# Optimization experiments

Hardware: AMD Instinct MI355X
Metric: run time of the kernel (lower is better)

Reference implementation:

```python
import jax, jax.numpy as jnp
import numpy as np

NMS_THR = 0.7
TOPK = 128      # fixed post-NMS rois per level (static padding for jit)
OUT = 14        # RoIAlign output size
SAMPLES = 2     # samples per bin per dim (fixed approximation of sampling_ratio=-1)
STRIDES = (32.0, 16.0, 8.0)


def get_channel(a):
    # a: [..., 4] boxes as (cx, cy, w, h); FPN level assignment, clamped to [1, 4]
    s = jnp.sqrt(a[..., 2] * a[..., 3])
    return jnp.clip(jnp.floor(3.0 + jnp.log2(s / 224.0)), 1.0, 4.0)


def cxcywh_to_xyxy(b):
    cx, cy, w, h = b[..., 0], b[..., 1], b[..., 2], b[..., 3]
    return jnp.stack([cx - w / 2, cy - h / 2, cx + w / 2, cy + h / 2], axis=-1)


def pairwise_iou(b):
    x1, y1, x2, y2 = b[:, 0], b[:, 1], b[:, 2], b[:, 3]
    area = jnp.maximum(x2 - x1, 0.0) * jnp.maximum(y2 - y1, 0.0)
    ix1 = jnp.maximum(x1[:, None], x1[None, :])
    iy1 = jnp.maximum(y1[:, None], y1[None, :])
    ix2 = jnp.minimum(x2[:, None], x2[None, :])
    iy2 = jnp.minimum(y2[:, None], y2[None, :])
    inter = jnp.maximum(ix2 - ix1, 0.0) * jnp.maximum(iy2 - iy1, 0.0)
    union = area[:, None] + area[None, :] - inter
    return inter / jnp.maximum(union, 1e-9)


def nms_keep(boxes_xyxy, scores, thr):
    # Greedy NMS over masked scores (-inf entries sort last and are excluded later).
    n = scores.shape[0]
    order = jnp.argsort(-scores)
    iou = pairwise_iou(boxes_xyxy[order])  # [N, N]
    idx = jnp.arange(n)

    def body(sup, i):
        keep_i = ~sup[i]
        sup = sup | (keep_i & (iou[i] > thr) & (idx > i))
        return sup, keep_i

    _, keeps_sorted = jax.lax.scan(body, jnp.zeros(n, dtype=bool), idx)
    return jnp.zeros(n, dtype=bool).at[order].set(keeps_sorted)


def roi_align(feat, boxes):
    # feat: [C, H, W]; boxes: [K, 4]. NOTE: the original prepare_boxes feeds
    # (cx, cy, w, h) straight into RoIAlign, which interprets them as
    # (x1, y1, x2, y2) -- replicated faithfully here. spatial_scale = 1.
    C, H, W = feat.shape
    K = boxes.shape[0]
    x1, y1, x2, y2 = boxes[:, 0], boxes[:, 1], boxes[:, 2], boxes[:, 3]
    rw = jnp.maximum(x2 - x1, 1.0)
    rh = jnp.maximum(y2 - y1, 1.0)
    bw = rw / OUT
    bh = rh / OUT
    # fractional bin offsets, [OUT*SAMPLES]
    f = (jnp.arange(OUT, dtype=feat.dtype)[:, None]
         + (jnp.arange(SAMPLES, dtype=feat.dtype)[None, :] + 0.5) / SAMPLES).reshape(-1)
    ys = y1[:, None] + bh[:, None] * f[None, :]  # [K, S]
    xs = x1[:, None] + bw[:, None] * f[None, :]
    Y = ys[:, :, None]  # [K, S, 1]
    X = xs[:, None, :]  # [K, 1, S]
    valid = (Y > -1.0) & (Y < H) & (X > -1.0) & (X < W)  # [K, S, S]
    Yc = jnp.clip(Y, 0.0, H - 1.0)
    Xc = jnp.clip(X, 0.0, W - 1.0)
    y0 = jnp.floor(Yc)
    x0 = jnp.floor(Xc)
    y0i = y0.astype(jnp.int32)
    x0i = x0.astype(jnp.int32)
    y1i = jnp.minimum(y0i + 1, H - 1)
    x1i = jnp.minimum(x0i + 1, W - 1)
    ly = Yc - y0
    lx = Xc - x0
    hy = 1.0 - ly
    hx = 1.0 - lx
    g = lambda yi, xi: feat[:, yi, xi]  # -> [C, K, S, S]
    val = (g(y0i, x0i) * (hy * hx) + g(y0i, x1i) * (hy * lx)
           + g(y1i, x0i) * (ly * hx) + g(y1i, x1i) * (ly * lx))
    val = val * valid.astype(val.dtype)
    val = val.reshape(C, K, OUT, SAMPLES, OUT, SAMPLES).mean(axis=(3, 5))
    return jnp.transpose(val, (1, 0, 2, 3))  # [K, C, OUT, OUT]


def level_extract(feat, boxes, scores, levs, nl):
    # one image, one target FPN level: mask, NMS, fixed top-K select, RoIAlign
    mask = levs == nl
    msc = jnp.where(mask, scores, -jnp.inf)
    xyxy = cxcywh_to_xyxy(boxes)
    keep = nms_keep(jax.lax.stop_gradient(xyxy), jax.lax.stop_gradient(msc), NMS_THR)
    eff = jnp.where(keep & mask, msc, -jnp.inf)
    vals, sel = jax.lax.top_k(jax.lax.stop_gradient(eff), TOPK)
    valid = jnp.isfinite(vals)
    rois = boxes[sel] * valid[:, None].astype(boxes.dtype)
    out = roi_align(feat, rois)
    return out * valid[:, None, None, None].astype(out.dtype)


def _forward(p32, p16, p8, p4, a32, a16, a8, s32, s16, s8):
    anchors = (a32, a16, a8)  # p4 proposals are computed then discarded in the
    # original (grouping loop only runs l in range(3)); p4 features are never
    # RoIAligned either (nl loops 1..3), so p4 only appears as an unused input.
    levs = jnp.concatenate([get_channel(a) for a in anchors], axis=1)      # [B, N]
    boxes = jnp.concatenate([a * s for a, s in zip(anchors, STRIDES)], axis=1)
    scores = jnp.concatenate([s32, s16, s8], axis=1)
    outs = []
    for nl, feat in zip((1.0, 2.0, 3.0), (p32, p16, p8)):
        fn = jax.vmap(lambda f, b, s, l, nl=nl: level_extract(f, b, s, l, nl))
        outs.append(fn(feat, boxes, scores, levs))  # [B, TOPK, C, 14, 14]
    return jnp.concatenate(outs, axis=1)  # [B, 3*TOPK, C, 14, 14]


def setup_inputs():
    key = jax.random.key(0)
    ks = jax.random.split(key, 10)
    B, C = 2, 256
    p32 = jax.random.normal(ks[0], (B, C, 32, 32), jnp.float32)
    p16 = jax.random.normal(ks[1], (B, C, 64, 64), jnp.float32)
    p8 = jax.random.normal(ks[2], (B, C, 128, 128), jnp.float32)
    p4 = jax.random.normal(ks[3], (B, C, 256, 256), jnp.float32)

    def mk_anchors(k, n, hf):
        k1, k2 = jax.random.split(k)
        cxy = jax.random.uniform(k1, (B, n, 2), jnp.float32) * hf
        wh = 16.0 + jax.random.uniform(k2, (B, n, 2), jnp.float32) * 434.0
        return jnp.concatenate([cxy, wh], axis=-1)

    anchors_32 = mk_anchors(ks[4], 512, 32.0)
    anchors_16 = mk_anchors(ks[5], 1024, 64.0)
    anchors_8 = mk_anchors(ks[6], 2048, 128.0)
    scores_32 = jax.random.normal(ks[7], (B, 512), jnp.float32)
    scores_16 = jax.random.normal(ks[8], (B, 1024), jnp.float32)
    scores_8 = jax.random.normal(ks[9], (B, 2048), jnp.float32)
    return dict(p32=p32, p16=p16, p8=p8, p4=p4,
                anchors_32=anchors_32, anchors_16=anchors_16, anchors_8=anchors_8,
                scores_32=scores_32, scores_16=scores_16, scores_8=scores_8)


def reference(p32, p16, p8, p4, anchors_32, anchors_16, anchors_8,
              scores_32, scores_16, scores_8):
    return _forward(p32, p16, p8, p4, anchors_32, anchors_16, anchors_8,
                    scores_32, scores_16, scores_8)
```

## Files before the change

### kernel.cpp

```cpp
#include <hip/hip_runtime.h>
#include <stdint.h>

#define NMS_THR 0.7f
#define TOPK 128
#define NTOT 3584
#define CAP 2048
#define OUTSZ 14
#define NSAMP 28

typedef unsigned long long u64;
typedef float vf4 __attribute__((ext_vector_type(4)));
typedef float float2u __attribute__((ext_vector_type(2), aligned(4)));

__device__ __forceinline__ u64 shfl_xor64(u64 v, int mask) {
    int lo = __shfl_xor((int)(unsigned)v, mask);
    int hi = __shfl_xor((int)(v >> 32), mask);
    return ((u64)(unsigned)hi << 32) | (unsigned)lo;
}
__device__ __forceinline__ void cex_shfl(u64 &e, int t, int j, int k) {
    u64 p = shfl_xor64(e, j);
    bool up = ((t & k) == 0);
    bool lower = ((t & j) == 0);
    u64 mn = (e < p) ? e : p;
    u64 mx = (e < p) ? p : e;
    e = (lower == up) ? mn : mx;
}
__device__ __forceinline__ void cex_reg(u64 &a, u64 &b, int t, int k) {
    bool up = ((t & k) == 0);
    if ((a > b) == up) { u64 x = a; a = b; b = x; }
}
__device__ __forceinline__ float boxarea(float4 b) {
    return __fmul_rn(fmaxf(__fsub_rn(b.z, b.x), 0.0f),
                     fmaxf(__fsub_rn(b.w, b.y), 0.0f));
}
__device__ __forceinline__ bool iou_gt(float4 a, float aa, float4 b, float ba) {
    float i1 = fmaxf(a.x, b.x), i2 = fmaxf(a.y, b.y);
    float i3 = fminf(a.z, b.z), i4 = fminf(a.w, b.w);
    float inr = __fmul_rn(fmaxf(__fsub_rn(i3, i1), 0.0f),
                          fmaxf(__fsub_rn(i4, i2), 0.0f));
    float unr = __fsub_rn(__fadd_rn(aa, ba), inr);
    return __fdiv_rn(inr, fmaxf(unr, 1e-9f)) > NMS_THR;
}

__device__ __forceinline__ void fetch_anchor(
    const float* __restrict__ a32, const float* __restrict__ a16,
    const float* __restrict__ a8,
    const float* __restrict__ s32, const float* __restrict__ s16,
    const float* __restrict__ s8,
    int b, int i, float* A, float* st, float* sc)
{
    const float* P;
    if (i < 512) {
        P = a32 + (b * 512 + i) * 4;  *st = 32.0f; *sc = s32[b * 512 + i];
    } else if (i < 1536) {
        int j = i - 512;
        P = a16 + (b * 1024 + j) * 4; *st = 16.0f; *sc = s16[b * 1024 + j];
    } else {
        int j = i - 1536;
        P = a8 + (b * 2048 + j) * 4;  *st = 8.0f;  *sc = s8[b * 2048 + j];
    }
    float4 v = *(const float4*)P;
    A[0] = v.x; A[1] = v.y; A[2] = v.z; A[3] = v.w;
}

__global__ __launch_bounds__(1024) void select_kernel(
    const float* __restrict__ a32, const float* __restrict__ a16,
    const float* __restrict__ a8,
    const float* __restrict__ s32, const float* __restrict__ s16,
    const float* __restrict__ s8,
    float* __restrict__ rois,
    int* __restrict__ validOut)
{
    __shared__ u64 keys[CAP];
    __shared__ float4 cbox4[CAP];
    __shared__ float4 kb4[TOPK];
    __shared__ float karea[TOPK];
    __shared__ u64 extw[16];
    __shared__ int selList[TOPK];
    __shared__ int mCount, keptSh;

    int prob = blockIdx.x;
    int b = prob / 3;
    int nl = prob % 3 + 1;
    int tid = threadIdx.x;
    int lane = tid & 63;
    int wv = tid >> 6;
    int t0 = (wv << 7) + lane;
    int t1 = t0 + 64;

    if (tid == 0) mCount = 0;
    __syncthreads();

    for (int i = tid; i < NTOT; i += 1024) {
        float A[4], st, sc;
        fetch_anchor(a32, a16, a8, s32, s16, s8, b, i, A, &st, &sc);
        float s = sqrtf(__fmul_rn(A[2], A[3]));
        float lv = floorf(__fadd_rn(3.0f, log2f(__fdiv_rn(s, 224.0f))));
        lv = fminf(fmaxf(lv, 1.0f), 4.0f);
        bool sel = ((int)lv == nl);
        u64 bal = __ballot(sel);
        if (bal) {
            int pos0;
            if (lane == 0) pos0 = atomicAdd(&mCount, __popcll(bal));
            pos0 = __shfl(pos0, 0);
            if (sel) {
                unsigned u = __float_as_uint(sc);
                u = (u & 0x80000000u) ? ~u : (u | 0x80000000u);
                unsigned d = ~u;
                int pos = pos0 + __popcll(bal & ((1ull << lane) - 1ull));
                if (pos < CAP) keys[pos] = ((u64)d << 32) | (unsigned)i;
            }
        }
    }
    __syncthreads();
    int m = mCount;
    if (m > CAP) m = CAP;
    for (int i = m + tid; i < CAP; i += 1024) keys[i] = ~0ull;
    __syncthreads();

    {
        u64 e0 = keys[t0], e1 = keys[t1];
        for (int k = 2; k <= 128; k <<= 1) {
            int jstart = k >> 1;
            if (k == 128) {
                cex_reg(e0, e1, t0, k);
                jstart = 32;
            }
            for (int j = jstart; j > 0; j >>= 1) {
                cex_shfl(e0, t0, j, k);
                cex_shfl(e1, t1, j, k);
            }
        }
        keys[t0] = e0; keys[t1] = e1;
    }
    __syncthreads();
    for (int k = 256; k <= 2048; k <<= 1) {
        for (int j = k >> 1; j >= 128; j >>= 1) {
            for (int t = tid; t < CAP; t += 1024) {
                int ixj = t ^ j;
                if (ixj > t) {
                    u64 a = keys[t], bb = keys[ixj];
                    bool up = ((t & k) == 0);
                    if ((a > bb) == up) { keys[t] = bb; keys[ixj] = a; }
                }
            }
            __syncthreads();
        }
        {
            u64 e0 = keys[t0], e1 = keys[t1];
            cex_reg(e0, e1, t0, k);
            for (int j = 32; j > 0; j >>= 1) {
                cex_shfl(e0, t0, j, k);
                cex_shfl(e1, t1, j, k);
            }
            keys[t0] = e0; keys[t1] = e1;
        }
        __syncthreads();
    }

    for (int r = tid; r < m; r += 1024) {
        int orig = (int)(keys[r] & 0xffffffffu);
        float A[4], st, sc;
        fetch_anchor(a32, a16, a8, s32, s16, s8, b, orig, A, &st, &sc);
        float cx = A[0] * st, cy = A[1] * st, w = A[2] * st, h = A[3] * st;
        float4 v;
        v.x = __fsub_rn(cx, 0.5f * w);
        v.y = __fsub_rn(cy, 0.5f * h);
        v.z = __fadd_rn(cx, 0.5f * w);
        v.w = __fadd_rn(cy, 0.5f * h);
        cbox4[r] = v;
    }
    __syncthreads();

    int kept = 0;
    for (int base = 0; base < m && kept < TOPK; base += 64) {
        int n = m - base; if (n > 64) n = 64;
        bool cv = lane < n;
        float4 cb = cbox4[base + (cv ? lane : 0)];
        float car = boxarea(cb);

        bool s = false;
        for (int kk = wv; kk < kept; kk += 16)
            if (iou_gt(kb4[kk], karea[kk], cb, car)) s = true;
        u64 balA = __ballot(s && cv);
        if (lane == 0) extw[wv] = balA;
        __syncthreads();

        if (wv == 0) {
            u64 ext = extw[0] | extw[1] | extw[2]  | extw[3]
                    | extw[4] | extw[5] | extw[6]  | extw[7]
                    | extw[8] | extw[9] | extw[10] | extw[11]
                    | extw[12]| extw[13]| extw[14] | extw[15];
            bool alive = cv && !((ext >> lane) & 1ull);
            int nk = kept;
            while (nk < TOPK) {
                u64 bal = __ballot(alive);
                if (bal == 0ull) break;
                int pick = __builtin_ctzll(bal);
                float4 pb;
                pb.x = __shfl(cb.x, pick);
                pb.y = __shfl(cb.y, pick);
                pb.z = __shfl(cb.z, pick);
                pb.w = __shfl(cb.w, pick);
                float par = __shfl(car, pick);
                if (lane == 0) selList[nk] = base + pick;
                if (lane == 1) { kb4[nk] = pb; karea[nk] = par; }
                alive = alive && (lane != pick) && !iou_gt(pb, par, cb, car);
                nk++;
            }
            if (lane == 0) keptSh = nk;
        }
        __syncthreads();
        kept = keptSh;
    }

    for (int k = tid; k < TOPK; k += 1024) {
        float4 rv = make_float4(0.0f, 0.0f, 0.0f, 0.0f);
        int vld = 0;
        if (k < kept) {
            int orig = (int)(keys[selList[k]] & 0xffffffffu);
            float A[4], st, sc;
            fetch_anchor(a32, a16, a8, s32, s16, s8, b, orig, A, &st, &sc);
            rv = make_float4(A[0] * st, A[1] * st, A[2] * st, A[3] * st);
            vld = 1;
        }
        ((float4*)rois)[prob * TOPK + k] = rv;
        validOut[prob * TOPK + k] = vld;
    }
}

__global__ __launch_bounds__(256) void roialign_kernel(
    const float* __restrict__ p32, const float* __restrict__ p16,
    const float* __restrict__ p8,
    const float* __restrict__ rois, const int* __restrict__ validIn,
    float* __restrict__ out)
{
    int roiIdx = blockIdx.x;
    int b = roiIdx / 384;
    int slot = roiIdx - b * 384;
    int lvl = slot / TOPK;
    int k = slot - lvl * TOPK;
    int prob = b * 3 + lvl;
    int tid = threadIdx.x;

    float* O = out + (size_t)roiIdx * 256 * 196;

    vf4 z = (vf4)0.0f;
    vf4* O4 = (vf4*)O;
    for (int i = tid; i < 12544; i += 256) O4[i] = z;

    int vld = validIn[prob * TOPK + k];
    if (!vld) return;

    int W;
    const float* feat;
    if (lvl == 0)      { W = 32;  feat = p32; }
    else if (lvl == 1) { W = 64;  feat = p16; }
    else               { W = 128; feat = p8; }
    int HW = W * W;
    const float* F0 = feat + (size_t)b * 256 * HW;

    __shared__ int sxb[NSAMP], sy0[NSAMP], sy1[NSAMP];
    __shared__ float swx0[NSAMP], swx1[NSAMP], shy[NSAMP], sly[NSAMP];
    __shared__ int sxv[NSAMP], syv[NSAMP];
    __shared__ int oiL[OUTSZ], ojL[OUTSZ];
    __shared__ int nyx[2];

    if (tid < 2 * NSAMP) {
        const float* R = rois + ((size_t)prob * TOPK + k) * 4;
        float x1 = R[0], y1 = R[1], x2 = R[2], y2 = R[3];
        float rw = fmaxf(__fsub_rn(x2, x1), 1.0f);
        float rh = fmaxf(__fsub_rn(y2, y1), 1.0f);
        float bw = __fdiv_rn(rw, 14.0f);
        float bh = __fdiv_rn(rh, 14.0f);
        int axis = tid / NSAMP;
        int s = tid - axis * NSAMP;
        float fi = (float)(s >> 1) + ((s & 1) ? 0.75f : 0.25f);
        float start = axis ? y1 : x1;
        float bsz = axis ? bh : bw;
        float lim = (float)W;
        float X = __fadd_rn(start, __fmul_rn(bsz, fi));
        bool v = (X > -1.0f) && (X < lim);
        float Xc = fminf(fmaxf(X, 0.0f), lim - 1.0f);
        float x0f = floorf(Xc);
        int x0 = (int)x0f;
        float l = __fsub_rn(Xc, x0f);
        float hh = __fsub_rn(1.0f, l);
        float vf = v ? 1.0f : 0.0f;
        if (axis == 0) {
            int base; float w0, w1;
            if (x0 >= W - 1) { base = W - 2; w0 = 0.0f; w1 = vf; }
            else             { base = x0;    w0 = hh * vf; w1 = l * vf; }
            sxb[s] = base; swx0[s] = w0; swx1[s] = w1; sxv[s] = v ? 1 : 0;
        } else {
            sy0[s] = x0; sy1[s] = min(x0 + 1, W - 1);
            shy[s] = hh * vf; sly[s] = l * vf; syv[s] = v ? 1 : 0;
        }
    }
    __syncthreads();

    if (tid == 0) {
        int n = 0;
        for (int oi = 0; oi < OUTSZ; oi++)
            if (syv[2 * oi] | syv[2 * oi + 1]) oiL[n++] = oi;
        nyx[0] = n;
    }
    if (tid == 1) {
        int n = 0;
        for (int oj = 0; oj < OUTSZ; oj++)
            if (sxv[2 * oj] | sxv[2 * oj + 1]) ojL[n++] = oj;
        nyx[1] = n;
    }
    __syncthreads();

    int ny = nyx[0], nx = nyx[1];
    int total = ny * nx;
    if (total == 0) return;

    int w = tid >> 6;
    int lane = tid & 63;

    for (int ci = w; ci < total; ci += 4) {
        int oi = oiL[ci / nx];
        int oj = ojL[ci - (ci / nx) * nx];
        int sA = oi * 2, sB = sA + 1;
        int tA = oj * 2, tB = tA + 1;
        int y0A = sy0[sA], y1A = sy1[sA], y0B = sy0[sB], y1B = sy1[sB];
        float hyA = shy[sA], lyA = sly[sA], hyB = shy[sB], lyB = sly[sB];
        int xA = sxb[tA], xB = sxb[tB];
        float xw0A = swx0[tA], xw1A = swx1[tA];
        float xw0B = swx0[tB], xw1B = swx1[tB];
        int p = oi * 14 + oj;

        for (int it = 0; it < 4; it++) {
            int c = lane + it * 64;
            const float* F = F0 + c * HW;
            const float* rA0 = F + y0A * W;
            const float* rA1 = F + y1A * W;
            const float* rB0 = F + y0B * W;
            const float* rB1 = F + y1B * W;

            float2u a0 = *(const float2u*)(rA0 + xA);
            float2u a1 = *(const float2u*)(rA1 + xA);
            float2u c0 = *(const float2u*)(rA0 + xB);
            float2u c1 = *(const float2u*)(rA1 + xB);
            float2u b0 = *(const float2u*)(rB0 + xA);
            float2u b1 = *(const float2u*)(rB1 + xA);
            float2u d0 = *(const float2u*)(rB0 + xB);
            float2u d1 = *(const float2u*)(rB1 + xB);

            float s00 = hyA * (xw0A * a0.x + xw1A * a0.y) + lyA * (xw0A * a1.x + xw1A * a1.y);
            float s01 = hyA * (xw0B * c0.x + xw1B * c0.y) + lyA * (xw0B * c1.x + xw1B * c1.y);
            float s10 = hyB * (xw0A * b0.x + xw1A * b0.y) + lyB * (xw0A * b1.x + xw1A * b1.y);
            float s11 = hyB * (xw0B * d0.x + xw1B * d0.y) + lyB * (xw0B * d1.x + xw1B * d1.y);
            O[c * 196 + p] = 0.25f * (s00 + s01 + s10 + s11);
        }
    }
}

extern "C" void kernel_launch(void* const* d_in, const int* in_sizes, int n_in,
                              void* d_out, int out_size, void* d_ws, size_t ws_size,
                              hipStream_t stream) {
    const float* p32 = (const float*)d_in[0];
    const float* p16 = (const float*)d_in[1];
    const float* p8  = (const float*)d_in[2];
    const float* a32 = (const float*)d_in[4];
    const float* a16 = (const float*)d_in[5];
    const float* a8  = (const float*)d_in[6];
    const float* s32 = (const float*)d_in[7];
    const float* s16 = (const float*)d_in[8];
    const float* s8  = (const float*)d_in[9];
    float* out = (float*)d_out;

    const size_t totalFloats = 3072 + 768;

    float* base;
    if (ws_size >= totalFloats * 4) {
        base = (float*)d_ws;
    } else {
        base = (float*)d_in[3];
    }
    float* rois  = base;
    int*   valid = (int*)(base + 3072);

    select_kernel<<<6, 1024, 0, stream>>>(a32, a16, a8, s32, s16, s8,
                                          rois, valid);
    roialign_kernel<<<768, 256, 0, stream>>>(p32, p16, p8, rois, valid, out);
}
```

Measured before the change: 348.1 us.

## Process NMS candidates in 256-wide chunks with 4 lane groups per round

The greedy NMS loop now takes 256 sorted candidates per round instead of 64. Four wave groups each cover 64 candidates and split the already-kept boxes four ways, which cuts the number of block-wide barrier rounds. Wave 0 then runs the serial pick over the four 64-lane sub-chunks in order, and each pick suppresses candidates in the later sub-chunks. The trade-off is more serial work for wave 0 per round, and some candidates past the last needed one may be tested needlessly once TOPK is reached.

```diff
diff --git a/kernel.cpp b/kernel.cpp
--- a/kernel.cpp
+++ b/kernel.cpp
@@ -173,41 +173,70 @@
     __syncthreads();
 
     int kept = 0;
-    for (int base = 0; base < m && kept < TOPK; base += 64) {
-        int n = m - base; if (n > 64) n = 64;
-        bool cv = lane < n;
-        float4 cb = cbox4[base + (cv ? lane : 0)];
+    int g = wv & 3;
+    int ks = wv >> 2;
+    for (int base = 0; base < m && kept < TOPK; base += 256) {
+        int n = m - base; if (n > 256) n = 256;
+
+        int c = g * 64 + lane;
+        bool cv = c < n;
+        float4 cb = cbox4[base + (cv ? c : 0)];
         float car = boxarea(cb);
-
         bool s = false;
-        for (int kk = wv; kk < kept; kk += 16)
+        for (int kk = ks; kk < kept; kk += 4)
             if (iou_gt(kb4[kk], karea[kk], cb, car)) s = true;
         u64 balA = __ballot(s && cv);
         if (lane == 0) extw[wv] = balA;
         __syncthreads();
 
         if (wv == 0) {
-            u64 ext = extw[0] | extw[1] | extw[2]  | extw[3]
-                    | extw[4] | extw[5] | extw[6]  | extw[7]
-                    | extw[8] | extw[9] | extw[10] | extw[11]
-                    | extw[12]| extw[13]| extw[14] | extw[15];
-            bool alive = cv && !((ext >> lane) & 1ull);
+            u64 e0 = extw[0] | extw[4] | extw[8]  | extw[12];
+            u64 e1 = extw[1] | extw[5] | extw[9]  | extw[13];
+            u64 e2 = extw[2] | extw[6] | extw[10] | extw[14];
+            u64 e3 = extw[3] | extw[7] | extw[11] | extw[15];
+            int c0 = lane, c1 = 64 + lane, c2 = 128 + lane, c3 = 192 + lane;
+            float4 B0 = cbox4[base + (c0 < n ? c0 : 0)];
+            float4 B1 = cbox4[base + (c1 < n ? c1 : 0)];
+            float4 B2 = cbox4[base + (c2 < n ? c2 : 0)];
+            float4 B3 = cbox4[base + (c3 < n ? c3 : 0)];
+            float a0 = boxarea(B0), a1 = boxarea(B1);
+            float a2 = boxarea(B2), a3 = boxarea(B3);
+            bool al0 = (c0 < n) && !((e0 >> lane) & 1ull);
+            bool al1 = (c1 < n) && !((e1 >> lane) & 1ull);
+            bool al2 = (c2 < n) && !((e2 >> lane) & 1ull);
+            bool al3 = (c3 < n) && !((e3 >> lane) & 1ull);
             int nk = kept;
-            while (nk < TOPK) {
-                u64 bal = __ballot(alive);
-                if (bal == 0ull) break;
-                int pick = __builtin_ctzll(bal);
-                float4 pb;
-                pb.x = __shfl(cb.x, pick);
-                pb.y = __shfl(cb.y, pick);
-                pb.z = __shfl(cb.z, pick);
-                pb.w = __shfl(cb.w, pick);
-                float par = __shfl(car, pick);
-                if (lane == 0) selList[nk] = base + pick;
-                if (lane == 1) { kb4[nk] = pb; karea[nk] = par; }
-                alive = alive && (lane != pick) && !iou_gt(pb, par, cb, car);
-                nk++;
-            }
+
+#define PICK_GROUP(AL, BB, AA, GOFF, KILL_LATER)                            \
+            while (nk < TOPK) {                                             \
+                u64 bal = __ballot(AL);                                     \
+                if (bal == 0ull) break;                                     \
+                int pick = __builtin_ctzll(bal);                            \
+                float4 pb;                                                  \
+                pb.x = __shfl(BB.x, pick);                                  \
+                pb.y = __shfl(BB.y, pick);                                  \
+                pb.z = __shfl(BB.z, pick);                                  \
+                pb.w = __shfl(BB.w, pick);                                  \
+                float par = __shfl(AA, pick);                               \
+                if (lane == 0) selList[nk] = base + GOFF + pick;            \
+                if (lane == 1) { kb4[nk] = pb; karea[nk] = par; }           \
+                AL = AL && (lane != pick) && !iou_gt(pb, par, BB, AA);      \
+                KILL_LATER                                                  \
+                nk++;                                                       \
+            }
+
+            PICK_GROUP(al0, B0, a0, 0,
+                al1 = al1 && !iou_gt(pb, par, B1, a1);
+                al2 = al2 && !iou_gt(pb, par, B2, a2);
+                al3 = al3 && !iou_gt(pb, par, B3, a3);)
+            PICK_GROUP(al1, B1, a1, 64,
+                al2 = al2 && !iou_gt(pb, par, B2, a2);
+                al3 = al3 && !iou_gt(pb, par, B3, a3);)
+            PICK_GROUP(al2, B2, a2, 128,
+                al3 = al3 && !iou_gt(pb, par, B3, a3);)
+            PICK_GROUP(al3, B3, a3, 192, )
+#undef PICK_GROUP
+
             if (lane == 0) keptSh = nk;
         }
         __syncthreads();
```

Result: slower. 362.8 us (+4.2%).
